# Performance work log

Hardware: AMD Instinct MI355X
Metric: run time of the kernel (lower is better)

## Reference

```python
import jax, jax.numpy as jnp
import numpy as np

EMBED_DIM = 1024
NUM_HEADS = 16
HEAD_DIM = EMBED_DIM // NUM_HEADS
FF_DIM = 4096
LN_EPS = 1e-5


def layer_norm(x, scale, bias):
    mu = jnp.mean(x, axis=-1, keepdims=True)
    var = jnp.mean(jnp.square(x - mu), axis=-1, keepdims=True)
    return (x - mu) * jax.lax.rsqrt(var + LN_EPS) * scale + bias


def setup_inputs() -> dict:
    key = jax.random.key(0)
    ks = jax.random.split(key, 9)
    E, F = EMBED_DIM, FF_DIM
    s = lambda d: 1.0 / np.sqrt(d)
    return {
        "x": jax.random.normal(ks[0], (2, 2048, E), dtype=jnp.float32),
        "qkv_w": jax.random.uniform(ks[1], (3 * E, E), jnp.float32, -s(E), s(E)),
        "out_w": jax.random.uniform(ks[2], (E, E), jnp.float32, -s(E), s(E)),
        "ff_up_w": jax.random.uniform(ks[3], (F, E), jnp.float32, -s(E), s(E)),
        "ff_down_w": jax.random.uniform(ks[4], (E, F), jnp.float32, -s(F), s(F)),
        "norm1_scale": jnp.ones((E,), jnp.float32),
        "norm1_bias": jnp.zeros((E,), jnp.float32),
        "norm2_scale": jnp.ones((E,), jnp.float32),
        "norm2_bias": jnp.zeros((E,), jnp.float32),
    }


def reference(x, qkv_w, out_w, ff_up_w, ff_down_w,
              norm1_scale, norm1_bias, norm2_scale, norm2_bias):
    B, S, E = x.shape
    H, D = NUM_HEADS, HEAD_DIM

    # --- attention sublayer ---
    residual = x
    h = layer_norm(x, norm1_scale, norm1_bias)
    qkv = h @ qkv_w.T                               # [B,S,3E]
    qkv = qkv.reshape(B, S, 3, H, D).transpose(2, 0, 3, 1, 4)  # [3,B,H,S,D]
    q, k, v = qkv[0], qkv[1], qkv[2]
    scores = jnp.einsum("bhqd,bhkd->bhqk", q, k) / np.sqrt(D)
    probs = jax.nn.softmax(scores, axis=-1)
    attn = jnp.einsum("bhqk,bhkd->bhqd", probs, v)  # [B,H,S,D]
    attn = attn.transpose(0, 2, 1, 3).reshape(B, S, E)
    x = residual + attn @ out_w.T

    # --- FFN sublayer ---
    residual = x
    h = layer_norm(x, norm2_scale, norm2_bias)
    h = jax.nn.gelu(h @ ff_up_w.T, approximate=False)
    h = h @ ff_down_w.T
    return residual + h
```

## Files before the change

kernel.cpp:

```cpp
#include <hip/hip_runtime.h>

typedef unsigned short u16;
typedef unsigned int u32;
typedef __attribute__((ext_vector_type(8))) short bf16x8;
typedef __attribute__((ext_vector_type(4))) float f32x4;

#define MFMA_BF16(a, b, c) __builtin_amdgcn_mfma_f32_16x16x32_bf16((a), (b), (c), 0, 0, 0)
#define BAR() __builtin_amdgcn_s_barrier()
#define WAITV(n) asm volatile("s_waitcnt vmcnt(" #n ")" ::: "memory")

#if __has_builtin(__builtin_amdgcn_exp2f)
#define EXP2(x) __builtin_amdgcn_exp2f(x)
#else
#define EXP2(x) exp2f(x)
#endif

__device__ __forceinline__ u16 f2bf(float f) {
    u32 u = __builtin_bit_cast(u32, f);
    u32 r = u + 0x7FFFu + ((u >> 16) & 1u);
    return (u16)(r >> 16);
}

__device__ __forceinline__ void gld16(const void* g, void* s) {
    __builtin_amdgcn_global_load_lds(
        (const __attribute__((address_space(1))) unsigned int*)g,
        (__attribute__((address_space(3))) unsigned int*)s, 16, 0, 0);
}

__global__ __launch_bounds__(256) void cvtall_k(const float* __restrict__ w0,
                                                const float* __restrict__ w1,
                                                const float* __restrict__ w2,
                                                const float* __restrict__ w3,
                                                u16* o0, u16* o1, u16* o2, u16* o3) {
    int j = blockIdx.x * 256 + threadIdx.x;
    const float* src; u16* dst;
    if (j < 786432)                       { src = w0; dst = o0; }
    else if ((j -= 786432) < 262144)      { src = w1; dst = o1; }
    else if ((j -= 262144) < 1048576)     { src = w2; dst = o2; }
    else { j -= 1048576;                    src = w3; dst = o3; }
    float4 v = ((const float4*)src)[j];
    ushort4 o;
    o.x = f2bf(v.x); o.y = f2bf(v.y); o.z = f2bf(v.z); o.w = f2bf(v.w);
    ((ushort4*)dst)[j] = o;
}

__global__ __launch_bounds__(256) void ln_k(const float* __restrict__ x,
                                            u16* __restrict__ out,
                                            const float* __restrict__ sc,
                                            const float* __restrict__ bi) {
    const int row = blockIdx.x;
    const int tid = threadIdx.x;
    const float4 v = ((const float4*)(x + (size_t)row * 1024))[tid];
    float s  = v.x + v.y + v.z + v.w;
    float s2 = v.x*v.x + v.y*v.y + v.z*v.z + v.w*v.w;
    #pragma unroll
    for (int m = 32; m; m >>= 1) { s += __shfl_xor(s, m); s2 += __shfl_xor(s2, m); }
    __shared__ float red[8];
    const int w = tid >> 6, l = tid & 63;
    if (l == 0) { red[w] = s; red[4 + w] = s2; }
    __syncthreads();
    s  = red[0] + red[1] + red[2] + red[3];
    s2 = red[4] + red[5] + red[6] + red[7];
    const float mu  = s * (1.0f / 1024.0f);
    const float var = s2 * (1.0f / 1024.0f) - mu * mu;
    const float rs  = rsqrtf(var + 1e-5f);
    const float4 sv = ((const float4*)sc)[tid];
    const float4 bv = ((const float4*)bi)[tid];
    ushort4 o;
    o.x = f2bf((v.x - mu) * rs * sv.x + bv.x);
    o.y = f2bf((v.y - mu) * rs * sv.y + bv.y);
    o.z = f2bf((v.z - mu) * rs * sv.z + bv.z);
    o.w = f2bf((v.w - mu) * rs * sv.w + bv.w);
    ((ushort4*)(out + (size_t)row * 1024))[tid] = o;
}

template<int NT, int EPI>
__global__ __launch_bounds__(512, 1) void gemm256_k(const u16* __restrict__ A,
                                                    const u16* __restrict__ B,
                                                    u16* __restrict__ Cb,
                                                    u16* __restrict__ vtout,
                                                    int M, int N, int K) {
    extern __shared__ u16 L[];
    const int tid = threadIdx.x;
    const int w = tid >> 6, l = tid & 63, g = l >> 4, lc = l & 15;
    const int wr = w >> 2, wc = w & 3;

    const int gx = gridDim.x, gy = gridDim.y;
    const int lin = blockIdx.x + gx * blockIdx.y;
    const int rx = gx >> 2, cy = gy >> 1;
    const int xcd = lin & 7, slot = lin >> 3;
    const int brow = (xcd & 3) * rx + (slot % rx);
    const int bcol = (xcd >> 2) * cy + (slot / rx);
    const int row0 = brow * 256, col0 = bcol * 256;

    const u16* gA = A + (size_t)row0 * K;
    const u16* gB = B + (size_t)col0 * K;
    int srow[4], soct[4];
    #pragma unroll
    for (int p = 0; p < 4; ++p) {
        const int idx = p * 512 + tid;
        srow[p] = idx >> 3;
        soct[p] = (idx & 7) ^ (srow[p] & 7);
    }

#define STG(t, p) do { \
        char* base_ = (char*)L + ((t) & 1) * 65536; \
        gld16(gA + (size_t)srow[p] * K + (size_t)(t) * 64 + soct[p] * 8, \
              base_ + ((p) * 512 + tid) * 16); \
        gld16(gB + (size_t)srow[p] * K + (size_t)(t) * 64 + soct[p] * 8, \
              base_ + 32768 + ((p) * 512 + tid) * 16); \
    } while (0)

    f32x4 acc[8][4] = {};

    STG(0, 0); STG(0, 1); STG(0, 2); STG(0, 3);

    const int ocx = lc & 7;

    for (int t = 0; t < NT; ++t) {
        const bool pf = (t + 1 < NT);
        if (pf) { STG(t + 1, 0); WAITV(2); } else { WAITV(0); }
        BAR();

        const u16* La = L + (t & 1) * 32768;
        const u16* Lb = La + 16384;

        bf16x8 bfr[4][2];
        #pragma unroll
        for (int j = 0; j < 4; ++j)
            #pragma unroll
            for (int kk = 0; kk < 2; ++kk)
                bfr[j][kk] = *(const bf16x8*)
                    &Lb[(wc * 64 + j * 16 + lc) * 64 + (((kk * 4 + g) ^ ocx) * 8)];

        #pragma unroll
        for (int ph = 0; ph < 4; ++ph) {
            if (ph == 2) BAR();
            bf16x8 af[2][2];
            #pragma unroll
            for (int ii = 0; ii < 2; ++ii)
                #pragma unroll
                for (int kk = 0; kk < 2; ++kk)
                    af[ii][kk] = *(const bf16x8*)
                        &La[(wr * 128 + (ph * 2 + ii) * 16 + lc) * 64 +
                            (((kk * 4 + g) ^ ocx) * 8)];
            __builtin_amdgcn_s_setprio(1);
            #pragma unroll
            for (int ii = 0; ii < 2; ++ii)
                #pragma unroll
                for (int j = 0; j < 4; ++j)
                    #pragma unroll
                    for (int kk = 0; kk < 2; ++kk)
                        acc[ph * 2 + ii][j] = MFMA_BF16(af[ii][kk], bfr[j][kk],
                                                        acc[ph * 2 + ii][j]);
            __builtin_amdgcn_s_setprio(0);
            if (pf && ph < 3) STG(t + 1, ph + 1);
        }
    }
#undef STG

    #pragma unroll
    for (int i = 0; i < 8; ++i)
        #pragma unroll
        for (int j = 0; j < 4; ++j) {
            const int rowb = row0 + wr * 128 + i * 16 + g * 4;
            const int col  = col0 + wc * 64 + j * 16 + lc;
            if (EPI == 0 && col >= 2048) {
                u32 lo, hi;
                asm("v_cvt_pk_bf16_f32 %0, %1, %2"
                    : "=v"(lo) : "v"(acc[i][j][0]), "v"(acc[i][j][1]));
                asm("v_cvt_pk_bf16_f32 %0, %1, %2"
                    : "=v"(hi) : "v"(acc[i][j][2]), "v"(acc[i][j][3]));
                const int hd = col - 2048, bb = rowb >> 11, token = rowb & 2047;
                uint2 pk; pk.x = lo; pk.y = hi;
                *(uint2*)(vtout + ((size_t)(bb * 16 + (hd >> 6)) * 64 + (hd & 63)) * 2048
                          + token) = pk;
            } else {
                #pragma unroll
                for (int r = 0; r < 4; ++r) {
                    const size_t off = (size_t)(rowb + r) * N + col;
                    const float v = acc[i][j][r];
                    if (EPI == 0) {
                        const float vv = (col < 1024) ? v * 0.180336880f : v;
                        Cb[off] = f2bf(vv);
                    } else {
                        const float u2 = fminf((v + 0.044715f * v * v * v)
                                               * 2.302118131f, 126.0f);
                        const float e = EXP2(u2);
                        Cb[off] = f2bf(v * e / (e + 1.0f));
                    }
                }
            }
        }
}

template<int NT>
__global__ __launch_bounds__(512, 1) void gemm128w8_k(const u16* __restrict__ A,
                                                      const u16* __restrict__ B,
                                                      float* __restrict__ Cf,
                                                      const float* __restrict__ resid,
                                                      int M, int N, int K) {
    extern __shared__ u16 L[];
    const int tid = threadIdx.x;
    const int w = tid >> 6, l = tid & 63, g = l >> 4, lc = l & 15;
    const int wr = w >> 1, wc = w & 1;
    const int row0 = blockIdx.x * 128, col0 = blockIdx.y * 128;

    const u16* gA = A + (size_t)row0 * K;
    const u16* gB = B + (size_t)col0 * K;
    const int srow = tid >> 3;
    const int soct = (tid & 7) ^ (srow & 7);

#define STG8(t) do { \
        char* base_ = (char*)L + ((t) & 3) * 32768; \
        _Pragma("unroll") \
        for (int p = 0; p < 4; ++p) { \
            const u16* src_ = (p < 2) ? gB : gA; \
            const int row_ = ((p & 1) << 6) + srow; \
            gld16(src_ + (size_t)row_ * K + (size_t)(t) * 64 + soct * 8, \
                  base_ + p * 8192 + tid * 16); \
        } \
    } while (0)

    f32x4 acc[2][4] = {};

    STG8(0); STG8(1); STG8(2);

    const int ocx = lc & 7;

    for (int t = 0; t < NT; ++t) {
        if      (t + 2 < NT) WAITV(8);
        else if (t + 1 < NT) WAITV(4);
        else                 WAITV(0);
        BAR();
        if (t + 3 < NT) STG8(t + 3);

        const u16* Lb = L + (t & 3) * 16384;
        const u16* La = Lb + 8192;

        bf16x8 bfr[4][2], af[2][2];
        #pragma unroll
        for (int j = 0; j < 4; ++j)
            #pragma unroll
            for (int kk = 0; kk < 2; ++kk)
                bfr[j][kk] = *(const bf16x8*)
                    &Lb[(wc * 64 + j * 16 + lc) * 64 + (((kk * 4 + g) ^ ocx) * 8)];
        #pragma unroll
        for (int ii = 0; ii < 2; ++ii)
            #pragma unroll
            for (int kk = 0; kk < 2; ++kk)
                af[ii][kk] = *(const bf16x8*)
                    &La[(wr * 32 + ii * 16 + lc) * 64 + (((kk * 4 + g) ^ ocx) * 8)];

        __builtin_amdgcn_s_setprio(1);
        #pragma unroll
        for (int ii = 0; ii < 2; ++ii)
            #pragma unroll
            for (int j = 0; j < 4; ++j)
                #pragma unroll
                for (int kk = 0; kk < 2; ++kk)
                    acc[ii][j] = MFMA_BF16(af[ii][kk], bfr[j][kk], acc[ii][j]);
        __builtin_amdgcn_s_setprio(0);
    }
#undef STG8

    #pragma unroll
    for (int i = 0; i < 2; ++i)
        #pragma unroll
        for (int j = 0; j < 4; ++j)
            #pragma unroll
            for (int r = 0; r < 4; ++r) {
                const int row = row0 + wr * 32 + i * 16 + g * 4 + r;
                const int col = col0 + wc * 64 + j * 16 + lc;
                const size_t off = (size_t)row * N + col;
                Cf[off] = acc[i][j][r] + resid[off];
            }
}

__global__ __launch_bounds__(512) void attn_k(const u16* __restrict__ qkv,
                                              const u16* __restrict__ vt,
                                              u16* __restrict__ ctx) {
    const int bh = blockIdx.x;
    const int qt = blockIdx.y;
    const int b = bh >> 4, h = bh & 15;
    const int tid = threadIdx.x, w = tid >> 6, l = tid & 63, g = l >> 4, lc = l & 15;
    const size_t tok0 = (size_t)b * 2048;

    const u16* Qg  = qkv + (tok0 + qt * 128) * 3072 + h * 64;
    const u16* Kg  = qkv + tok0 * 3072 + 1024 + h * 64;
    const u16* Vtg = vt + (size_t)bh * 64 * 2048;

    __shared__ u16 Ks[2][64 * 64];
    __shared__ u16 Vts[2][64 * 64];
    __shared__ u16 QPs[128 * 64];
    u16* Pw = QPs + w * 1024;

    {
        const int q0r = tid >> 3,         q0c = (tid & 7) ^ (q0r & 7);
        const int q1r = (tid + 512) >> 3, q1c = ((tid + 512) & 7) ^ (q1r & 7);
        gld16(Qg + (size_t)q0r * 3072 + q0c * 8, (char*)QPs + tid * 16);
        gld16(Qg + (size_t)q1r * 3072 + q1c * 8, (char*)QPs + (tid + 512) * 16);
    }
    const int skr = tid >> 3, skc = (tid & 7) ^ (skr & 7);
    const u16* kp = Kg + (size_t)skr * 3072 + skc * 8;
    const u16* vp = Vtg + (size_t)skr * 2048 + skc * 8;
    gld16(kp, (char*)Ks[0] + tid * 16);
    gld16(vp, (char*)Vts[0] + tid * 16);
    kp += 64 * 3072; vp += 64;
    __syncthreads();

    bf16x8 qf[2];
    {
        const int qrow = w * 16 + lc;
        qf[0] = *(const bf16x8*)&QPs[qrow * 64 + ((g       ^ (lc & 7)) * 8)];
        qf[1] = *(const bf16x8*)&QPs[qrow * 64 + (((4 + g) ^ (lc & 7)) * 8)];
    }

    f32x4 oacc[4] = {};
    float mrow = -1e30f, lrow = 0.0f;
    const int hsw = (lc & 7) << 3;

    for (int kt = 0; kt < 32; ++kt) {
        WAITV(0);
        BAR();
        if (kt + 1 < 32) {
            gld16(kp, (char*)Ks[(kt + 1) & 1] + tid * 16);
            gld16(vp, (char*)Vts[(kt + 1) & 1] + tid * 16);
            kp += 64 * 3072; vp += 64;
        }
        const u16* Kc = Ks[kt & 1];
        const u16* Vc = Vts[kt & 1];

        f32x4 sacc[4] = {};
        __builtin_amdgcn_s_setprio(1);
        #pragma unroll
        for (int kk = 0; kk < 2; ++kk)
            #pragma unroll
            for (int nt = 0; nt < 4; ++nt) {
                const int krow = nt * 16 + lc;
                const bf16x8 kb = *(const bf16x8*)
                    &Kc[krow * 64 + (((kk * 4 + g) ^ (lc & 7)) * 8)];
                sacc[nt] = MFMA_BF16(kb, qf[kk], sacc[nt]);
            }
        __builtin_amdgcn_s_setprio(0);

        float mx;
        {
            const float* sv = (const float*)sacc;
            float m = sv[0];
            #pragma unroll
            for (int q = 0; q < 7; ++q) {
                float t;
                asm("v_max3_f32 %0, %1, %2, %3"
                    : "=v"(t) : "v"(m), "v"(sv[2 * q + 1]), "v"(sv[2 * q + 2]));
                m = t;
            }
            mx = fmaxf(m, sv[15]);
        }
        mx = fmaxf(mx, __shfl_xor(mx, 16));
        mx = fmaxf(mx, __shfl_xor(mx, 32));
        const bool ru = __any(mx > mrow + 8.0f);
        float corr = 1.0f;
        if (ru) {
            const float mnew = fmaxf(mrow, mx);
            corr = EXP2(mrow - mnew);
            mrow = mnew;
        }

        float p[4][4];
        float ps = 0.0f;
        #pragma unroll
        for (int nt = 0; nt < 4; ++nt)
            #pragma unroll
            for (int r = 0; r < 4; ++r) {
                const float pv = EXP2(sacc[nt][r] - mrow);
                p[nt][r] = pv;
                ps += pv;
            }
        ps += __shfl_xor(ps, 16);
        ps += __shfl_xor(ps, 32);

        #pragma unroll
        for (int nt = 0; nt < 4; ++nt) {
            uint2 pk;
            asm("v_cvt_pk_bf16_f32 %0, %1, %2" : "=v"(pk.x) : "v"(p[nt][0]), "v"(p[nt][1]));
            asm("v_cvt_pk_bf16_f32 %0, %1, %2" : "=v"(pk.y) : "v"(p[nt][2]), "v"(p[nt][3]));
            *(uint2*)&Pw[lc * 64 + ((nt * 16 + g * 4) ^ hsw)] = pk;
        }

        if (ru) {
            lrow = lrow * corr + ps;
            float cq[4];
            #pragma unroll
            for (int r = 0; r < 4; ++r) cq[r] = __shfl(corr, g * 4 + r);
            #pragma unroll
            for (int nt = 0; nt < 4; ++nt)
                #pragma unroll
                for (int r = 0; r < 4; ++r) oacc[nt][r] *= cq[r];
        } else {
            lrow += ps;
        }

        __builtin_amdgcn_s_setprio(1);
        #pragma unroll
        for (int kk = 0; kk < 2; ++kk) {
            const bf16x8 pa = *(const bf16x8*)
                &Pw[lc * 64 + ((kk * 32 + g * 8) ^ hsw)];
            #pragma unroll
            for (int nt = 0; nt < 4; ++nt) {
                const int vrow = nt * 16 + lc;
                const bf16x8 vb = *(const bf16x8*)
                    &Vc[vrow * 64 + (((kk * 4 + g) ^ (lc & 7)) * 8)];
                oacc[nt] = MFMA_BF16(pa, vb, oacc[nt]);
            }
        }
        __builtin_amdgcn_s_setprio(0);
    }

    float lq[4];
    #pragma unroll
    for (int r = 0; r < 4; ++r) lq[r] = 1.0f / __shfl(lrow, g * 4 + r);
    #pragma unroll
    for (int nt = 0; nt < 4; ++nt)
        #pragma unroll
        for (int r = 0; r < 4; ++r) {
            const float o = oacc[nt][r] * lq[r];
            const size_t token = tok0 + qt * 128 + w * 16 + g * 4 + r;
            ctx[token * 1024 + h * 64 + nt * 16 + lc] = f2bf(o);
        }
}

extern "C" void kernel_launch(void* const* d_in, const int* in_sizes, int n_in,
                              void* d_out, int out_size, void* d_ws, size_t ws_size,
                              hipStream_t stream) {
    const float* x      = (const float*)d_in[0];
    const float* qkv_w  = (const float*)d_in[1];
    const float* out_w  = (const float*)d_in[2];
    const float* up_w   = (const float*)d_in[3];
    const float* down_w = (const float*)d_in[4];
    const float* n1s    = (const float*)d_in[5];
    const float* n1b    = (const float*)d_in[6];
    const float* n2s    = (const float*)d_in[7];
    const float* n2b    = (const float*)d_in[8];
    float* out = (float*)d_out;

    char* ws = (char*)d_ws;
    size_t off = 0;
    auto alloc = [&](size_t bytes) -> void* {
        void* p = ws + off;
        off += (bytes + 255) & ~(size_t)255;
        return p;
    };
    u16*   qkvw_b = (u16*)alloc(3072ull * 1024 * 2);
    u16*   outw_b = (u16*)alloc(1024ull * 1024 * 2);
    u16*   upw_b  = (u16*)alloc(4096ull * 1024 * 2);
    u16*   dnw_b  = (u16*)alloc(1024ull * 4096 * 2);
    u16*   h_b    = (u16*)alloc(4096ull * 1024 * 2);
    u16*   qkv_o  = (u16*)alloc(4096ull * 3072 * 2);
    u16*   ctx    = (u16*)alloc(4096ull * 1024 * 2);
    float* x2     = (float*)alloc(4096ull * 1024 * 4);
    u16*   u      = (u16*)alloc(4096ull * 4096 * 2);
    u16*   vt     = u;

    hipFuncSetAttribute((const void*)&gemm256_k<16, 0>,
                        hipFuncAttributeMaxDynamicSharedMemorySize, 131072);
    hipFuncSetAttribute((const void*)&gemm256_k<16, 2>,
                        hipFuncAttributeMaxDynamicSharedMemorySize, 131072);
    hipFuncSetAttribute((const void*)&gemm128w8_k<16>,
                        hipFuncAttributeMaxDynamicSharedMemorySize, 131072);
    hipFuncSetAttribute((const void*)&gemm128w8_k<64>,
                        hipFuncAttributeMaxDynamicSharedMemorySize, 131072);

    cvtall_k<<<12288, 256, 0, stream>>>(qkv_w, out_w, up_w, down_w,
                                        qkvw_b, outw_b, upw_b, dnw_b);

    ln_k<<<4096, 256, 0, stream>>>(x, h_b, n1s, n1b);
    gemm256_k<16, 0><<<dim3(16, 12), 512, 131072, stream>>>(h_b, qkvw_b, qkv_o, vt,
                                                            4096, 3072, 1024);
    attn_k<<<dim3(32, 16), 512, 0, stream>>>(qkv_o, vt, ctx);
    gemm128w8_k<16><<<dim3(32, 8), 512, 131072, stream>>>(ctx, outw_b, x2, x,
                                                          4096, 1024, 1024);

    ln_k<<<4096, 256, 0, stream>>>(x2, h_b, n2s, n2b);
    gemm256_k<16, 2><<<dim3(16, 16), 512, 131072, stream>>>(h_b, upw_b, u, nullptr,
                                                            4096, 4096, 1024);
    gemm128w8_k<64><<<dim3(32, 8), 512, 131072, stream>>>(u, dnw_b, out, x2,
                                                          4096, 1024, 4096);
}
```

Before: 200.7 us.

## Switch attention to 32x32x16 MFMA with 4 waves of 32 query rows

The attention kernel now uses 32x32x16 bf16 MFMA instructions instead of 16x16x32. Each of 4 waves (256 threads, down from 8 waves) owns 32 query rows rather than 16, and the K/V tile loads are split across two loads per thread. The larger MFMA shape is meant to raise arithmetic intensity per LDS fragment read and cut per-wave softmax and shuffle overhead. The cost is fewer waves per block and more accumulator registers per wave, which can hurt latency hiding and occupancy.

```diff
diff --git a/kernel.cpp b/kernel.cpp
--- a/kernel.cpp
+++ b/kernel.cpp
@@ -4,8 +4,10 @@
 typedef unsigned int u32;
 typedef __attribute__((ext_vector_type(8))) short bf16x8;
 typedef __attribute__((ext_vector_type(4))) float f32x4;
+typedef __attribute__((ext_vector_type(16))) float f32x16;
 
 #define MFMA_BF16(a, b, c) __builtin_amdgcn_mfma_f32_16x16x32_bf16((a), (b), (c), 0, 0, 0)
+#define MFMA32(a, b, c) __builtin_amdgcn_mfma_f32_32x32x16_bf16((a), (b), (c), 0, 0, 0)
 #define BAR() __builtin_amdgcn_s_barrier()
 #define WAITV(n) asm volatile("s_waitcnt vmcnt(" #n ")" ::: "memory")
 
@@ -277,13 +279,14 @@
             }
 }
 
-__global__ __launch_bounds__(512) void attn_k(const u16* __restrict__ qkv,
+__global__ __launch_bounds__(256) void attn_k(const u16* __restrict__ qkv,
                                               const u16* __restrict__ vt,
                                               u16* __restrict__ ctx) {
     const int bh = blockIdx.x;
     const int qt = blockIdx.y;
     const int b = bh >> 4, h = bh & 15;
-    const int tid = threadIdx.x, w = tid >> 6, l = tid & 63, g = l >> 4, lc = l & 15;
+    const int tid = threadIdx.x, w = tid >> 6, l = tid & 63;
+    const int lo = l & 31, hi = l >> 5;
     const size_t tok0 = (size_t)b * 2048;
 
     const u16* Qg  = qkv + (tok0 + qt * 128) * 3072 + h * 64;
@@ -293,71 +296,82 @@
     __shared__ u16 Ks[2][64 * 64];
     __shared__ u16 Vts[2][64 * 64];
     __shared__ u16 QPs[128 * 64];
-    u16* Pw = QPs + w * 1024;
-
+    u16* Pw = QPs + w * 2048;
+
+    #pragma unroll
+    for (int c = 0; c < 4; ++c) {
+        const int idx = c * 256 + tid;
+        const int qr = idx >> 3, qc = (idx & 7) ^ (qr & 7);
+        gld16(Qg + (size_t)qr * 3072 + qc * 8, (char*)QPs + idx * 16);
+    }
+    const int s0r = tid >> 3,         s0c = (tid & 7) ^ (s0r & 7);
+    const int s1r = (tid + 256) >> 3, s1c = ((tid + 256) & 7) ^ (s1r & 7);
+    const u16* kp0 = Kg + (size_t)s0r * 3072 + s0c * 8;
+    const u16* kp1 = Kg + (size_t)s1r * 3072 + s1c * 8;
+    const u16* vp0 = Vtg + (size_t)s0r * 2048 + s0c * 8;
+    const u16* vp1 = Vtg + (size_t)s1r * 2048 + s1c * 8;
+    gld16(kp0, (char*)Ks[0] + tid * 16);
+    gld16(kp1, (char*)Ks[0] + (tid + 256) * 16);
+    gld16(vp0, (char*)Vts[0] + tid * 16);
+    gld16(vp1, (char*)Vts[0] + (tid + 256) * 16);
+    kp0 += 64 * 3072; kp1 += 64 * 3072; vp0 += 64; vp1 += 64;
+    __syncthreads();
+
+    bf16x8 qf[4];
     {
-        const int q0r = tid >> 3,         q0c = (tid & 7) ^ (q0r & 7);
-        const int q1r = (tid + 512) >> 3, q1c = ((tid + 512) & 7) ^ (q1r & 7);
-        gld16(Qg + (size_t)q0r * 3072 + q0c * 8, (char*)QPs + tid * 16);
-        gld16(Qg + (size_t)q1r * 3072 + q1c * 8, (char*)QPs + (tid + 512) * 16);
+        const int qrow = w * 32 + lo;
+        #pragma unroll
+        for (int kk = 0; kk < 4; ++kk)
+            qf[kk] = *(const bf16x8*)
+                &QPs[qrow * 64 + (((kk * 2 + hi) ^ (qrow & 7)) * 8)];
     }
-    const int skr = tid >> 3, skc = (tid & 7) ^ (skr & 7);
-    const u16* kp = Kg + (size_t)skr * 3072 + skc * 8;
-    const u16* vp = Vtg + (size_t)skr * 2048 + skc * 8;
-    gld16(kp, (char*)Ks[0] + tid * 16);
-    gld16(vp, (char*)Vts[0] + tid * 16);
-    kp += 64 * 3072; vp += 64;
-    __syncthreads();
-
-    bf16x8 qf[2];
-    {
-        const int qrow = w * 16 + lc;
-        qf[0] = *(const bf16x8*)&QPs[qrow * 64 + ((g       ^ (lc & 7)) * 8)];
-        qf[1] = *(const bf16x8*)&QPs[qrow * 64 + (((4 + g) ^ (lc & 7)) * 8)];
-    }
-
-    f32x4 oacc[4] = {};
+
+    f32x16 oacc[2] = {};
     float mrow = -1e30f, lrow = 0.0f;
-    const int hsw = (lc & 7) << 3;
+    const int psw = lo & 7;
 
     for (int kt = 0; kt < 32; ++kt) {
         WAITV(0);
         BAR();
         if (kt + 1 < 32) {
-            gld16(kp, (char*)Ks[(kt + 1) & 1] + tid * 16);
-            gld16(vp, (char*)Vts[(kt + 1) & 1] + tid * 16);
-            kp += 64 * 3072; vp += 64;
+            char* kd = (char*)Ks[(kt + 1) & 1];
+            char* vd = (char*)Vts[(kt + 1) & 1];
+            gld16(kp0, kd + tid * 16);
+            gld16(kp1, kd + (tid + 256) * 16);
+            gld16(vp0, vd + tid * 16);
+            gld16(vp1, vd + (tid + 256) * 16);
+            kp0 += 64 * 3072; kp1 += 64 * 3072; vp0 += 64; vp1 += 64;
         }
         const u16* Kc = Ks[kt & 1];
         const u16* Vc = Vts[kt & 1];
 
-        f32x4 sacc[4] = {};
+        f32x16 sacc[2] = {};
         __builtin_amdgcn_s_setprio(1);
         #pragma unroll
-        for (int kk = 0; kk < 2; ++kk)
-            #pragma unroll
-            for (int nt = 0; nt < 4; ++nt) {
-                const int krow = nt * 16 + lc;
-                const bf16x8 kb = *(const bf16x8*)
-                    &Kc[krow * 64 + (((kk * 4 + g) ^ (lc & 7)) * 8)];
-                sacc[nt] = MFMA_BF16(kb, qf[kk], sacc[nt]);
+        for (int kb = 0; kb < 2; ++kb) {
+            const int krow = kb * 32 + lo;
+            #pragma unroll
+            for (int kk = 0; kk < 4; ++kk) {
+                const bf16x8 kf = *(const bf16x8*)
+                    &Kc[krow * 64 + (((kk * 2 + hi) ^ (krow & 7)) * 8)];
+                sacc[kb] = MFMA32(kf, qf[kk], sacc[kb]);
             }
+        }
         __builtin_amdgcn_s_setprio(0);
 
+        const float* sv = (const float*)sacc;
         float mx;
         {
-            const float* sv = (const float*)sacc;
             float m = sv[0];
             #pragma unroll
-            for (int q = 0; q < 7; ++q) {
+            for (int q = 0; q < 15; ++q) {
                 float t;
                 asm("v_max3_f32 %0, %1, %2, %3"
                     : "=v"(t) : "v"(m), "v"(sv[2 * q + 1]), "v"(sv[2 * q + 2]));
                 m = t;
             }
-            mx = fmaxf(m, sv[15]);
-        }
-        mx = fmaxf(mx, __shfl_xor(mx, 16));
+            mx = fmaxf(m, sv[31]);
+        }
         mx = fmaxf(mx, __shfl_xor(mx, 32));
         const bool ru = __any(mx > mrow + 8.0f);
         float corr = 1.0f;
@@ -367,66 +381,70 @@
             mrow = mnew;
         }
 
-        float p[4][4];
+        float p[32];
         float ps = 0.0f;
         #pragma unroll
-        for (int nt = 0; nt < 4; ++nt)
-            #pragma unroll
-            for (int r = 0; r < 4; ++r) {
-                const float pv = EXP2(sacc[nt][r] - mrow);
-                p[nt][r] = pv;
-                ps += pv;
+        for (int i = 0; i < 32; ++i) {
+            const float pv = EXP2(sv[i] - mrow);
+            p[i] = pv;
+            ps += pv;
+        }
+        ps += __shfl_xor(ps, 32);
+
+        #pragma unroll
+        for (int kb = 0; kb < 2; ++kb)
+            #pragma unroll
+            for (int j = 0; j < 4; ++j) {
+                uint2 pk;
+                asm("v_cvt_pk_bf16_f32 %0, %1, %2"
+                    : "=v"(pk.x) : "v"(p[kb * 16 + 4 * j]), "v"(p[kb * 16 + 4 * j + 1]));
+                asm("v_cvt_pk_bf16_f32 %0, %1, %2"
+                    : "=v"(pk.y) : "v"(p[kb * 16 + 4 * j + 2]), "v"(p[kb * 16 + 4 * j + 3]));
+                *(uint2*)&Pw[lo * 64 + (((kb * 4 + j) ^ psw) * 8) + hi * 4] = pk;
             }
-        ps += __shfl_xor(ps, 16);
-        ps += __shfl_xor(ps, 32);
-
-        #pragma unroll
-        for (int nt = 0; nt < 4; ++nt) {
-            uint2 pk;
-            asm("v_cvt_pk_bf16_f32 %0, %1, %2" : "=v"(pk.x) : "v"(p[nt][0]), "v"(p[nt][1]));
-            asm("v_cvt_pk_bf16_f32 %0, %1, %2" : "=v"(pk.y) : "v"(p[nt][2]), "v"(p[nt][3]));
-            *(uint2*)&Pw[lc * 64 + ((nt * 16 + g * 4) ^ hsw)] = pk;
-        }
 
         if (ru) {
             lrow = lrow * corr + ps;
-            float cq[4];
-            #pragma unroll
-            for (int r = 0; r < 4; ++r) cq[r] = __shfl(corr, g * 4 + r);
-            #pragma unroll
-            for (int nt = 0; nt < 4; ++nt)
+            float cq[16];
+            #pragma unroll
+            for (int r = 0; r < 16; ++r)
+                cq[r] = __shfl(corr, (r & 3) + 8 * (r >> 2) + 4 * hi);
+            #pragma unroll
+            for (int db = 0; db < 2; ++db)
                 #pragma unroll
-                for (int r = 0; r < 4; ++r) oacc[nt][r] *= cq[r];
+                for (int r = 0; r < 16; ++r) oacc[db][r] *= cq[r];
         } else {
             lrow += ps;
         }
 
         __builtin_amdgcn_s_setprio(1);
         #pragma unroll
-        for (int kk = 0; kk < 2; ++kk) {
-            const bf16x8 pa = *(const bf16x8*)
-                &Pw[lc * 64 + ((kk * 32 + g * 8) ^ hsw)];
-            #pragma unroll
-            for (int nt = 0; nt < 4; ++nt) {
-                const int vrow = nt * 16 + lc;
-                const bf16x8 vb = *(const bf16x8*)
-                    &Vc[vrow * 64 + (((kk * 4 + g) ^ (lc & 7)) * 8)];
-                oacc[nt] = MFMA_BF16(pa, vb, oacc[nt]);
+        for (int kkk = 0; kkk < 4; ++kkk) {
+            const bf16x8 pf = *(const bf16x8*)
+                &Pw[lo * 64 + (((kkk * 2 + hi) ^ psw) * 8)];
+            #pragma unroll
+            for (int db = 0; db < 2; ++db) {
+                const int drow = db * 32 + lo;
+                const bf16x8 vf = *(const bf16x8*)
+                    &Vc[drow * 64 + (((kkk * 2 + hi) ^ (drow & 7)) * 8)];
+                oacc[db] = MFMA32(pf, vf, oacc[db]);
             }
         }
         __builtin_amdgcn_s_setprio(0);
     }
 
-    float lq[4];
-    #pragma unroll
-    for (int r = 0; r < 4; ++r) lq[r] = 1.0f / __shfl(lrow, g * 4 + r);
-    #pragma unroll
-    for (int nt = 0; nt < 4; ++nt)
-        #pragma unroll
-        for (int r = 0; r < 4; ++r) {
-            const float o = oacc[nt][r] * lq[r];
-            const size_t token = tok0 + qt * 128 + w * 16 + g * 4 + r;
-            ctx[token * 1024 + h * 64 + nt * 16 + lc] = f2bf(o);
+    float lq[16];
+    #pragma unroll
+    for (int r = 0; r < 16; ++r)
+        lq[r] = 1.0f / __shfl(lrow, (r & 3) + 8 * (r >> 2) + 4 * hi);
+    #pragma unroll
+    for (int db = 0; db < 2; ++db)
+        #pragma unroll
+        for (int r = 0; r < 16; ++r) {
+            const float o = oacc[db][r] * lq[r];
+            const int qrow = (r & 3) + 8 * (r >> 2) + 4 * hi;
+            const size_t token = tok0 + qt * 128 + w * 32 + qrow;
+            ctx[token * 1024 + h * 64 + db * 32 + lo] = f2bf(o);
         }
 }
 
@@ -477,7 +495,7 @@
     ln_k<<<4096, 256, 0, stream>>>(x, h_b, n1s, n1b);
     gemm256_k<16, 0><<<dim3(16, 12), 512, 131072, stream>>>(h_b, qkvw_b, qkv_o, vt,
                                                             4096, 3072, 1024);
-    attn_k<<<dim3(32, 16), 512, 0, stream>>>(qkv_o, vt, ctx);
+    attn_k<<<dim3(32, 16), 256, 0, stream>>>(qkv_o, vt, ctx);
     gemm128w8_k<16><<<dim3(32, 8), 512, 131072, stream>>>(ctx, outw_b, x2, x,
                                                           4096, 1024, 1024);
 
```

After: 208.2 us. 3.7% more time.
